# Performance work log

Measured on AMD Instinct MI355X. Metric: run time of the kernel, lower is better.

Reference implementation:

```python
import jax, jax.numpy as jnp
import numpy as np

K = 2
HD = 1024
IN = 784
NPARAMS = K + 2**K - 1  # 5
TRIL_R = np.array([0, 1, 1])  # tril_indices(2,2)
TRIL_C = np.array([0, 0, 1])


def setup_inputs() -> dict:
    key = jax.random.key(0)
    ks = jax.random.split(key, 8)
    B, T = 4096, 32
    s = 0.02
    return {
        "x": jax.random.normal(ks[0], (B, IN), jnp.float32),
        "hx": jnp.zeros((B, HD), jnp.float32),
        "eps": jax.random.normal(ks[1], (T, B, K), jnp.float32),
        "W_ih": jax.random.normal(ks[2], (HD, IN), jnp.float32) * s,
        "b_ih": jax.random.normal(ks[3], (HD,), jnp.float32) * s,
        "W_hh": jax.random.normal(ks[4], (HD, HD), jnp.float32) * s,
        "b_hh": jax.random.normal(ks[5], (HD,), jnp.float32) * s,
        "fe_W": jax.random.normal(ks[6], (NPARAMS, HD), jnp.float32) * s,
        "fe_b": jax.random.normal(ks[7], (NPARAMS,), jnp.float32) * s,
        "num_ticks": T,
    }


def _forward(x, hx, eps, W_ih, b_ih, W_hh, b_hh, fe_W, fe_b):
    B = x.shape[0]
    x_proj = x @ W_ih.T + b_ih  # invariant across ticks: [B, HD]
    diag = jnp.arange(K)

    def step(h, eps_t):
        h = jnp.tanh(x_proj + h @ W_hh.T + b_hh)  # RNNCell
        fe = h @ fe_W.T + fe_b                    # [B, NPARAMS]
        mus = fe[:, :K]
        sigmas = fe[:, K:]
        L = jnp.zeros((B, K, K), fe.dtype).at[:, TRIL_R, TRIL_C].set(sigmas)
        L = L.at[:, diag, diag].set(jax.nn.softplus(L[:, diag, diag]))
        z = mus + jnp.einsum('bij,bj->bi', L, eps_t)  # reparameterized sample
        return h, (z, L)

    _, (zs, Ls) = jax.lax.scan(step, hx, eps)  # zs: [T,B,K], Ls: [T,B,K,K]
    zs = jnp.transpose(zs, (1, 2, 0))          # [B, K, T]
    Ls = jnp.transpose(Ls, (1, 2, 3, 0))       # [B, K, K, T]
    # NOTE: original code stacks all_zs for both `zs` and `mus` (faithful to source).
    return zs, zs, Ls


def reference(x, hx, eps, W_ih, b_ih, W_hh, b_hh, fe_W, fe_b, num_ticks):
    eps = eps[:num_ticks]
    return _forward(x, hx, eps, W_ih, b_ih, W_hh, b_hh, fe_W, fe_b)
```

## Files before the change

### kernel.cpp

```cpp
#include <hip/hip_runtime.h>
#include <hip/hip_bf16.h>
#include <stdint.h>

#define B_ROWS 4096
#define HD 1024
#define IN_DIM 784
#define IN_PAD 832
#define NEXT 1152
#define T_TICKS 32

typedef float f32x4 __attribute__((ext_vector_type(4)));
typedef short short8 __attribute__((ext_vector_type(8)));
typedef __hip_bfloat16 bf16;

__device__ __forceinline__ float b2f(short s) {
  unsigned u = ((unsigned)(unsigned short)s) << 16;
  float f; __builtin_memcpy(&f, &u, 4); return f;
}

__device__ __forceinline__ float softplus_f(float x) {
  if (x > 20.f) return x;
  return log1pf(expf(x));
}

__device__ __forceinline__ float tanh_fast(float x) {
  x = fminf(fmaxf(x, -15.f), 15.f);
  float e = __expf(2.f * x);
  return (e - 1.f) / (e + 1.f);
}

__device__ __forceinline__ void gload_lds16(const void* g, void* l) {
  __builtin_amdgcn_global_load_lds(
      (const __attribute__((address_space(1))) uint32_t*)g,
      (__attribute__((address_space(3))) uint32_t*)l, 16, 0, 0);
}

__global__ __launch_bounds__(256) void conv_pad_kernel(
    const float* __restrict__ src, bf16* __restrict__ dst,
    int rows, int scols, int dcols) {
  int idx = blockIdx.x * 256 + threadIdx.x;
  int total = rows * dcols;
  if (idx >= total) return;
  int r = idx / dcols, c = idx - r * dcols;
  float v = (c < scols) ? src[(size_t)r * scols + c] : 0.f;
  dst[idx] = __float2bfloat16(v);
}

__global__ __launch_bounds__(256) void build_whhext(
    const float* __restrict__ Whh, const float* __restrict__ feW,
    bf16* __restrict__ dst) {
  int idx = blockIdx.x * 256 + threadIdx.x;
  if (idx >= NEXT * HD) return;
  int r = idx / HD, c = idx - r * HD;
  float v = 0.f;
  if (r < HD) v = Whh[(size_t)r * HD + c];
  else if (r < HD + 5) v = feW[(size_t)(r - HD) * HD + c];
  dst[idx] = __float2bfloat16(v);
}

template<int KDIM, int MODE, int NT>
__global__ __launch_bounds__(256) void gemm_bt(
    const bf16* __restrict__ A, int ldaB,
    const bf16* __restrict__ Bw, int ldbB,
    const float* __restrict__ bias1, const float* __restrict__ bias2,
    const bf16* __restrict__ xp, bf16* __restrict__ xp_out,
    bf16* __restrict__ outH, float* __restrict__ feRaw, int tprev)
{
  __shared__ bf16 lA[2][64 * 64];
  __shared__ bf16 lB[2][128 * 64];
  const int tid = threadIdx.x;
  const int lane = tid & 63, w = tid >> 6;
  const int wm = w & 1, wn = w >> 1;
  const int l3 = lane >> 3, l7 = lane & 7;
  const int gcol = l7 ^ l3;
  const int r = lane & 15, q = lane >> 4;
  const int r7 = r & 7;

  int bid = blockIdx.x;
  int mx, ny;
  if (NT == 8) {
    int v = (bid & 7) * 64 + (bid >> 3);
    mx = v >> 3; ny = v & 7;
  } else {
    int v = (bid & 7) * 72 + (bid >> 3);
    mx = v / 9; ny = v - mx * 9;
  }
  const int bm0 = mx * 64, bn0 = ny * 128;

  f32x4 acc[2][4] = {};

  const char* Asrc = (const char*)A + (size_t)(bm0 + l3) * ldaB + gcol * 16;
  const char* Bsrc = (const char*)Bw + (size_t)(bn0 + l3) * ldbB + gcol * 16;
  char* lAb0 = (char*)&lA[0][0];
  char* lBb0 = (char*)&lB[0][0];

  const int NK = KDIM / 64;

#define STAGE(buf, kt)                                                         \
  {                                                                            \
    const char* Ak = Asrc + (kt) * 128;                                        \
    const char* Bk = Bsrc + (kt) * 128;                                        \
    _Pragma("unroll") for (int j = 0; j < 2; ++j) {                            \
      int iA = w * 2 + j;                                                      \
      gload_lds16(Ak + (size_t)iA * 8 * ldaB, lAb0 + (buf) * 8192 + iA * 1024);\
    }                                                                          \
    _Pragma("unroll") for (int j = 0; j < 4; ++j) {                            \
      int iB = w * 4 + j;                                                      \
      gload_lds16(Bk + (size_t)iB * 8 * ldbB, lBb0 + (buf) * 16384 + iB * 1024);\
    }                                                                          \
  }

  STAGE(0, 0);
  int cur = 0;

  for (int kt = 0; kt < NK; ++kt) {
    if (kt + 1 < NK) {
      STAGE(cur ^ 1, kt + 1);
      asm volatile("s_waitcnt vmcnt(6)" ::: "memory");
    } else {
      asm volatile("s_waitcnt vmcnt(0)" ::: "memory");
    }
    __builtin_amdgcn_s_barrier();

    const char* lAb = lAb0 + cur * 8192;
    const char* lBb = lBb0 + cur * 16384;
    short8 af[2][2], bfr[2][4];
#pragma unroll
    for (int ks = 0; ks < 2; ++ks) {
      int cc = ks * 4 + q;
      int sw = (cc ^ r7) << 4;
#pragma unroll
      for (int m = 0; m < 2; ++m) {
        int row = wm * 32 + m * 16 + r;
        af[ks][m] = *(const short8*)(lAb + row * 128 + sw);
      }
#pragma unroll
      for (int n = 0; n < 4; ++n) {
        int row = wn * 64 + n * 16 + r;
        bfr[ks][n] = *(const short8*)(lBb + row * 128 + sw);
      }
    }
    asm volatile("s_waitcnt lgkmcnt(0)" ::: "memory");
    __builtin_amdgcn_s_barrier();
    __builtin_amdgcn_sched_barrier(0);

#pragma unroll
    for (int ks = 0; ks < 2; ++ks)
#pragma unroll
      for (int m = 0; m < 2; ++m)
#pragma unroll
        for (int n = 0; n < 4; ++n)
          acc[m][n] = __builtin_amdgcn_mfma_f32_16x16x32_bf16(af[ks][m], bfr[ks][n], acc[m][n], 0, 0, 0);

    cur ^= 1;
  }
#undef STAGE

#pragma unroll
  for (int m = 0; m < 2; ++m) {
#pragma unroll
    for (int n = 0; n < 4; ++n) {
      int coll = wn * 64 + n * 16 + r;
      int col = bn0 + coll;
#pragma unroll
      for (int i = 0; i < 4; ++i) {
        int row = bm0 + wm * 32 + m * 16 + q * 4 + i;
        float v = acc[m][n][i];
        if (MODE == 0) {
          xp_out[(size_t)row * HD + col] = __float2bfloat16(v + bias1[col] + bias2[col]);
        } else {
          if (NT == 9 && ny == 8) {
            if (coll < 5 && tprev >= 0)
              feRaw[((size_t)row * T_TICKS + tprev) * 5 + coll] = v;
          } else {
            float val = tanh_fast(v + b2f(*(const short*)&xp[(size_t)row * HD + col]));
            outH[(size_t)row * HD + col] = __float2bfloat16(val);
          }
        }
      }
    }
  }
}

__global__ __launch_bounds__(256) void fe_last(
    const bf16* __restrict__ h, const float* __restrict__ feW,
    float* __restrict__ feRaw)
{
  int wid = threadIdx.x >> 6, lane = threadIdx.x & 63;
  int b = blockIdx.x * 4 + wid;
  const bf16* hr = h + (size_t)b * HD + lane * 16;
  short8 hv0 = *(const short8*)hr;
  short8 hv1 = *(const short8*)(hr + 8);
  float hvf[16];
#pragma unroll
  for (int e = 0; e < 8; ++e) { hvf[e] = b2f(hv0[e]); hvf[8 + e] = b2f(hv1[e]); }

  float a0 = 0, a1 = 0, a2 = 0, a3 = 0, a4 = 0;
  int col0 = lane * 16;
#pragma unroll
  for (int e = 0; e < 16; ++e) {
    float hv = hvf[e];
    int col = col0 + e;
    a0 += hv * feW[0 * HD + col];
    a1 += hv * feW[1 * HD + col];
    a2 += hv * feW[2 * HD + col];
    a3 += hv * feW[3 * HD + col];
    a4 += hv * feW[4 * HD + col];
  }
#pragma unroll
  for (int off = 32; off >= 1; off >>= 1) {
    a0 += __shfl_xor(a0, off);
    a1 += __shfl_xor(a1, off);
    a2 += __shfl_xor(a2, off);
    a3 += __shfl_xor(a3, off);
    a4 += __shfl_xor(a4, off);
  }
  if (lane == 0) {
    float* fr = feRaw + ((size_t)b * T_TICKS + (T_TICKS - 1)) * 5;
    fr[0] = a0; fr[1] = a1; fr[2] = a2; fr[3] = a3; fr[4] = a4;
  }
}

__global__ __launch_bounds__(256) void finish_kernel(
    const float* __restrict__ feRaw, const float* __restrict__ feB,
    const float* __restrict__ eps, float* __restrict__ out)
{
  int gid = blockIdx.x * 256 + threadIdx.x;
  if (gid >= B_ROWS * T_TICKS) return;
  int b = gid >> 5, t = gid & 31;
  const float* fr = feRaw + ((size_t)b * T_TICKS + t) * 5;
  float mu0 = fr[0] + feB[0], mu1 = fr[1] + feB[1];
  float L00 = softplus_f(fr[2] + feB[2]);
  float L10 = fr[3] + feB[3];
  float L11 = softplus_f(fr[4] + feB[4]);
  const float* ep = eps + ((size_t)t * B_ROWS + b) * 2;
  float e0 = ep[0], e1 = ep[1];
  float z0 = mu0 + L00 * e0;
  float z1 = mu1 + L10 * e0 + L11 * e1;

  float* zs0 = out;
  float* zs1 = out + (size_t)B_ROWS * 2 * T_TICKS;
  float* Ls  = out + (size_t)2 * B_ROWS * 2 * T_TICKS;
  size_t zb = (size_t)b * 2 * T_TICKS + t;
  zs0[zb] = z0; zs0[zb + T_TICKS] = z1;
  zs1[zb] = z0; zs1[zb + T_TICKS] = z1;
  size_t lb = (size_t)b * 4 * T_TICKS + t;
  Ls[lb] = L00;
  Ls[lb + T_TICKS] = 0.f;
  Ls[lb + 2 * T_TICKS] = L10;
  Ls[lb + 3 * T_TICKS] = L11;
}

extern "C" void kernel_launch(void* const* d_in, const int* in_sizes, int n_in,
                              void* d_out, int out_size, void* d_ws, size_t ws_size,
                              hipStream_t stream) {
  const float* x    = (const float*)d_in[0];
  const float* hx   = (const float*)d_in[1];
  const float* eps  = (const float*)d_in[2];
  const float* W_ih = (const float*)d_in[3];
  const float* b_ih = (const float*)d_in[4];
  const float* W_hh = (const float*)d_in[5];
  const float* b_hh = (const float*)d_in[6];
  const float* fe_W = (const float*)d_in[7];
  const float* fe_b = (const float*)d_in[8];
  float* out = (float*)d_out;

  char* ws = (char*)d_ws;
  bf16* x_bf    = (bf16*)ws;  ws += (size_t)B_ROWS * IN_PAD * 2;
  bf16* wih_bf  = (bf16*)ws;  ws += (size_t)HD * IN_PAD * 2;
  bf16* whhe_bf = (bf16*)ws;  ws += (size_t)NEXT * HD * 2;
  bf16* xp_bf   = (bf16*)ws;  ws += (size_t)B_ROWS * HD * 2;
  bf16* hA = (bf16*)ws;       ws += (size_t)B_ROWS * HD * 2;
  bf16* hB = (bf16*)ws;       ws += (size_t)B_ROWS * HD * 2;
  float* feRaw = (float*)ws;  ws += (size_t)B_ROWS * T_TICKS * 5 * 4;

  conv_pad_kernel<<<(B_ROWS * IN_PAD + 255) / 256, 256, 0, stream>>>(x, x_bf, B_ROWS, IN_DIM, IN_PAD);
  conv_pad_kernel<<<(HD * IN_PAD + 255) / 256, 256, 0, stream>>>(W_ih, wih_bf, HD, IN_DIM, IN_PAD);
  build_whhext<<<(NEXT * HD + 255) / 256, 256, 0, stream>>>(W_hh, fe_W, whhe_bf);
  conv_pad_kernel<<<(B_ROWS * HD + 255) / 256, 256, 0, stream>>>(hx, hA, B_ROWS, HD, HD);

  gemm_bt<IN_PAD, 0, 8><<<512, 256, 0, stream>>>(
      x_bf, IN_PAD * 2, wih_bf, IN_PAD * 2, b_ih, b_hh,
      nullptr, xp_bf, nullptr, nullptr, -1);

  for (int t = 0; t < T_TICKS; ++t) {
    const bf16* hin = (t & 1) ? hB : hA;
    bf16* hout      = (t & 1) ? hA : hB;
    gemm_bt<HD, 1, 9><<<576, 256, 0, stream>>>(
        hin, HD * 2, whhe_bf, HD * 2, nullptr, nullptr,
        xp_bf, nullptr, hout, feRaw, t - 1);
  }
  fe_last<<<B_ROWS / 4, 256, 0, stream>>>(hA, fe_W, feRaw);
  finish_kernel<<<(B_ROWS * T_TICKS + 255) / 256, 256, 0, stream>>>(feRaw, fe_b, eps, out);
}
```

Before: 720.0 us.

## Fold fe projection into wave 0 of per-tick GEMM and triple-buffer LDS

The extra ninth column tile that computed the fe projection as a padded GEMM block is removed. Wave 0 of the blocks with ny<4 now does a small 16x16 MFMA against a padded fe_W tile, reusing the A tile already in LDS, so each tick launches 512 blocks instead of 576. The K loop also moves from double to triple buffering, with two stages kept in flight. The cost is more LDS per block, which may lower occupancy, plus extra load and MFMA work on wave 0 of half the blocks.

Result: faster. 576.8 us (-19.9%).

```diff
diff --git a/kernel.cpp b/kernel.cpp
--- a/kernel.cpp
+++ b/kernel.cpp
@@ -6,12 +6,15 @@
 #define HD 1024
 #define IN_DIM 784
 #define IN_PAD 832
-#define NEXT 1152
 #define T_TICKS 32
 
 typedef float f32x4 __attribute__((ext_vector_type(4)));
 typedef short short8 __attribute__((ext_vector_type(8)));
 typedef __hip_bfloat16 bf16;
+
+#define BUF_SZ 24576
+#define FEW_OFF (3 * BUF_SZ)
+#define LDS_TOTAL (3 * BUF_SZ + 3 * 2048)
 
 __device__ __forceinline__ float b2f(short s) {
   unsigned u = ((unsigned)(unsigned short)s) << 16;
@@ -46,28 +49,31 @@
   dst[idx] = __float2bfloat16(v);
 }
 
-__global__ __launch_bounds__(256) void build_whhext(
+__global__ __launch_bounds__(256) void build_wext(
     const float* __restrict__ Whh, const float* __restrict__ feW,
-    bf16* __restrict__ dst) {
+    bf16* __restrict__ whh_bf, bf16* __restrict__ feWp) {
   int idx = blockIdx.x * 256 + threadIdx.x;
-  if (idx >= NEXT * HD) return;
+  if (idx >= (HD + 16) * HD) return;
   int r = idx / HD, c = idx - r * HD;
-  float v = 0.f;
-  if (r < HD) v = Whh[(size_t)r * HD + c];
-  else if (r < HD + 5) v = feW[(size_t)(r - HD) * HD + c];
-  dst[idx] = __float2bfloat16(v);
-}
-
-template<int KDIM, int MODE, int NT>
+  if (r < HD) {
+    whh_bf[idx] = __float2bfloat16(Whh[(size_t)r * HD + c]);
+  } else {
+    int fr = r - HD;
+    float v = (fr < 5) ? feW[(size_t)fr * HD + c] : 0.f;
+    feWp[(size_t)fr * HD + c] = __float2bfloat16(v);
+  }
+}
+
+template<int KDIM, int MODE>
 __global__ __launch_bounds__(256) void gemm_bt(
-    const bf16* __restrict__ A, int ldaB,
-    const bf16* __restrict__ Bw, int ldbB,
+    const bf16* __restrict__ A,
+    const bf16* __restrict__ Bw,
+    const bf16* __restrict__ feWp,
     const float* __restrict__ bias1, const float* __restrict__ bias2,
     const bf16* __restrict__ xp, bf16* __restrict__ xp_out,
     bf16* __restrict__ outH, float* __restrict__ feRaw, int tprev)
 {
-  __shared__ bf16 lA[2][64 * 64];
-  __shared__ bf16 lB[2][128 * 64];
+  __shared__ char lds[LDS_TOTAL];
   const int tid = threadIdx.x;
   const int lane = tid & 63, w = tid >> 6;
   const int wm = w & 1, wn = w >> 1;
@@ -75,56 +81,69 @@
   const int gcol = l7 ^ l3;
   const int r = lane & 15, q = lane >> 4;
   const int r7 = r & 7;
+  const int ldaB = KDIM * 2, ldbB = KDIM * 2;
 
   int bid = blockIdx.x;
-  int mx, ny;
-  if (NT == 8) {
-    int v = (bid & 7) * 64 + (bid >> 3);
-    mx = v >> 3; ny = v & 7;
-  } else {
-    int v = (bid & 7) * 72 + (bid >> 3);
-    mx = v / 9; ny = v - mx * 9;
-  }
+  int v = (bid & 7) * 64 + (bid >> 3);
+  const int mx = v >> 3, ny = v & 7;
   const int bm0 = mx * 64, bn0 = ny * 128;
 
+  const bool feB = (MODE == 1) && (ny < 4);
+  const bool feW0 = feB && (w == 0);
+
   f32x4 acc[2][4] = {};
+  f32x4 acc_fe = {};
 
   const char* Asrc = (const char*)A + (size_t)(bm0 + l3) * ldaB + gcol * 16;
   const char* Bsrc = (const char*)Bw + (size_t)(bn0 + l3) * ldbB + gcol * 16;
-  char* lAb0 = (char*)&lA[0][0];
-  char* lBb0 = (char*)&lB[0][0];
+  const char* Fsrc = (const char*)feWp + (size_t)l3 * 2048 + gcol * 16;
 
   const int NK = KDIM / 64;
 
-#define STAGE(buf, kt)                                                         \
-  {                                                                            \
-    const char* Ak = Asrc + (kt) * 128;                                        \
-    const char* Bk = Bsrc + (kt) * 128;                                        \
-    _Pragma("unroll") for (int j = 0; j < 2; ++j) {                            \
-      int iA = w * 2 + j;                                                      \
-      gload_lds16(Ak + (size_t)iA * 8 * ldaB, lAb0 + (buf) * 8192 + iA * 1024);\
-    }                                                                          \
-    _Pragma("unroll") for (int j = 0; j < 4; ++j) {                            \
-      int iB = w * 4 + j;                                                      \
-      gload_lds16(Bk + (size_t)iB * 8 * ldbB, lBb0 + (buf) * 16384 + iB * 1024);\
-    }                                                                          \
+#define STAGE(buf, kt)                                                          \
+  {                                                                             \
+    const char* Ak = Asrc + (kt) * 128;                                         \
+    const char* Bk = Bsrc + (kt) * 128;                                         \
+    _Pragma("unroll") for (int j = 0; j < 2; ++j) {                             \
+      int iA = w * 2 + j;                                                       \
+      gload_lds16(Ak + (size_t)iA * 8 * ldaB, lds + (buf) * BUF_SZ + iA * 1024);\
+    }                                                                           \
+    _Pragma("unroll") for (int j = 0; j < 4; ++j) {                             \
+      int iB = w * 4 + j;                                                       \
+      gload_lds16(Bk + (size_t)iB * 8 * ldbB,                                   \
+                  lds + (buf) * BUF_SZ + 8192 + iB * 1024);                     \
+    }                                                                           \
+    if (feW0) {                                                                 \
+      const char* Fk = Fsrc + (kt) * 128;                                       \
+      _Pragma("unroll") for (int j = 0; j < 2; ++j) {                           \
+        gload_lds16(Fk + (size_t)j * 8 * 2048,                                  \
+                    lds + FEW_OFF + (buf) * 2048 + j * 1024);                   \
+      }                                                                         \
+    }                                                                           \
   }
 
   STAGE(0, 0);
-  int cur = 0;
+  STAGE(1, 1);
+  int b0 = 0;
 
   for (int kt = 0; kt < NK; ++kt) {
-    if (kt + 1 < NK) {
-      STAGE(cur ^ 1, kt + 1);
-      asm volatile("s_waitcnt vmcnt(6)" ::: "memory");
+    int bs = b0 + 2; if (bs >= 3) bs -= 3;
+    if (kt + 2 < NK) {
+      STAGE(bs, kt + 2);
+      if (feW0) asm volatile("s_waitcnt vmcnt(16)" ::: "memory");
+      else      asm volatile("s_waitcnt vmcnt(12)" ::: "memory");
+    } else if (kt + 2 == NK) {
+      if (feW0) asm volatile("s_waitcnt vmcnt(8)" ::: "memory");
+      else      asm volatile("s_waitcnt vmcnt(6)" ::: "memory");
     } else {
       asm volatile("s_waitcnt vmcnt(0)" ::: "memory");
     }
     __builtin_amdgcn_s_barrier();
-
-    const char* lAb = lAb0 + cur * 8192;
-    const char* lBb = lBb0 + cur * 16384;
-    short8 af[2][2], bfr[2][4];
+    __builtin_amdgcn_sched_barrier(0);
+
+    const char* lAb = lds + b0 * BUF_SZ;
+    const char* lBb = lAb + 8192;
+    short8 af[2][2], bfr[2][4], af_fe[2], bf_fe[2];
 #pragma unroll
     for (int ks = 0; ks < 2; ++ks) {
       int cc = ks * 4 + q;
@@ -140,6 +159,15 @@
         bfr[ks][n] = *(const short8*)(lBb + row * 128 + sw);
       }
     }
+    if (feW0) {
+      const char* lFb = lds + FEW_OFF + b0 * 2048;
+#pragma unroll
+      for (int ks = 0; ks < 2; ++ks) {
+        int sw = ((ks * 4 + q) ^ r7) << 4;
+        af_fe[ks] = *(const short8*)(lAb + (ny * 16 + r) * 128 + sw);
+        bf_fe[ks] = *(const short8*)(lFb + r * 128 + sw);
+      }
+    }
     asm volatile("s_waitcnt lgkmcnt(0)" ::: "memory");
     __builtin_amdgcn_s_barrier();
     __builtin_amdgcn_sched_barrier(0);
@@ -151,8 +179,12 @@
 #pragma unroll
         for (int n = 0; n < 4; ++n)
           acc[m][n] = __builtin_amdgcn_mfma_f32_16x16x32_bf16(af[ks][m], bfr[ks][n], acc[m][n], 0, 0, 0);
-
-    cur ^= 1;
+    if (feW0) {
+      acc_fe = __builtin_amdgcn_mfma_f32_16x16x32_bf16(af_fe[0], bf_fe[0], acc_fe, 0, 0, 0);
+      acc_fe = __builtin_amdgcn_mfma_f32_16x16x32_bf16(af_fe[1], bf_fe[1], acc_fe, 0, 0, 0);
+    }
+
+    if (++b0 == 3) b0 = 0;
   }
 #undef STAGE
 
@@ -160,24 +192,25 @@
   for (int m = 0; m < 2; ++m) {
 #pragma unroll
     for (int n = 0; n < 4; ++n) {
-      int coll = wn * 64 + n * 16 + r;
-      int col = bn0 + coll;
+      int col = bn0 + wn * 64 + n * 16 + r;
 #pragma unroll
       for (int i = 0; i < 4; ++i) {
         int row = bm0 + wm * 32 + m * 16 + q * 4 + i;
-        float v = acc[m][n][i];
+        float vv = acc[m][n][i];
         if (MODE == 0) {
-          xp_out[(size_t)row * HD + col] = __float2bfloat16(v + bias1[col] + bias2[col]);
+          xp_out[(size_t)row * HD + col] = __float2bfloat16(vv + bias1[col] + bias2[col]);
         } else {
-          if (NT == 9 && ny == 8) {
-            if (coll < 5 && tprev >= 0)
-              feRaw[((size_t)row * T_TICKS + tprev) * 5 + coll] = v;
-          } else {
-            float val = tanh_fast(v + b2f(*(const short*)&xp[(size_t)row * HD + col]));
-            outH[(size_t)row * HD + col] = __float2bfloat16(val);
-          }
+          float val = tanh_fast(vv + b2f(*(const short*)&xp[(size_t)row * HD + col]));
+          outH[(size_t)row * HD + col] = __float2bfloat16(val);
         }
       }
+    }
+  }
+  if (MODE == 1 && feW0 && tprev >= 0 && r < 5) {
+#pragma unroll
+    for (int i = 0; i < 4; ++i) {
+      int rowg = bm0 + ny * 16 + q * 4 + i;
+      feRaw[((size_t)rowg * T_TICKS + tprev) * 5 + r] = acc_fe[i];
     }
   }
 }
@@ -268,7 +301,8 @@
   char* ws = (char*)d_ws;
   bf16* x_bf    = (bf16*)ws;  ws += (size_t)B_ROWS * IN_PAD * 2;
   bf16* wih_bf  = (bf16*)ws;  ws += (size_t)HD * IN_PAD * 2;
-  bf16* whhe_bf = (bf16*)ws;  ws += (size_t)NEXT * HD * 2;
+  bf16* whh_bf  = (bf16*)ws;  ws += (size_t)HD * HD * 2;
+  bf16* feWp    = (bf16*)ws;  ws += (size_t)16 * HD * 2;
   bf16* xp_bf   = (bf16*)ws;  ws += (size_t)B_ROWS * HD * 2;
   bf16* hA = (bf16*)ws;       ws += (size_t)B_ROWS * HD * 2;
   bf16* hB = (bf16*)ws;       ws += (size_t)B_ROWS * HD * 2;
@@ -276,18 +310,18 @@
 
   conv_pad_kernel<<<(B_ROWS * IN_PAD + 255) / 256, 256, 0, stream>>>(x, x_bf, B_ROWS, IN_DIM, IN_PAD);
   conv_pad_kernel<<<(HD * IN_PAD + 255) / 256, 256, 0, stream>>>(W_ih, wih_bf, HD, IN_DIM, IN_PAD);
-  build_whhext<<<(NEXT * HD + 255) / 256, 256, 0, stream>>>(W_hh, fe_W, whhe_bf);
+  build_wext<<<((HD + 16) * HD + 255) / 256, 256, 0, stream>>>(W_hh, fe_W, whh_bf, feWp);
   conv_pad_kernel<<<(B_ROWS * HD + 255) / 256, 256, 0, stream>>>(hx, hA, B_ROWS, HD, HD);
 
-  gemm_bt<IN_PAD, 0, 8><<<512, 256, 0, stream>>>(
-      x_bf, IN_PAD * 2, wih_bf, IN_PAD * 2, b_ih, b_hh,
+  gemm_bt<IN_PAD, 0><<<512, 256, 0, stream>>>(
+      x_bf, wih_bf, nullptr, b_ih, b_hh,
       nullptr, xp_bf, nullptr, nullptr, -1);
 
   for (int t = 0; t < T_TICKS; ++t) {
     const bf16* hin = (t & 1) ? hB : hA;
     bf16* hout      = (t & 1) ? hA : hB;
-    gemm_bt<HD, 1, 9><<<576, 256, 0, stream>>>(
-        hin, HD * 2, whhe_bf, HD * 2, nullptr, nullptr,
+    gemm_bt<HD, 1><<<512, 256, 0, stream>>>(
+        hin, whh_bf, feWp, nullptr, nullptr,
         xp_bf, nullptr, hout, feRaw, t - 1);
   }
   fe_last<<<B_ROWS / 4, 256, 0, stream>>>(hA, fe_W, feRaw);
```

## Pre-pack weights into MFMA fragment layout and load B directly to registers

Applied to the files above, without the earlier changes.

Weights are repacked once into an MFMA-fragment-ordered layout so each wave loads its B operands straight from global memory into registers with coalesced 16-byte loads, double-buffered two k-steps ahead, and only the A tile goes through LDS. The extra 9th column tile that computed the 5 fe outputs is removed. The fe projection is now done by wave 0 of blocks with ny<4 using a small packed fe weight block and one extra MFMA pair per k-step, so the recurrent launch drops from 576 to 512 blocks. This cuts LDS traffic and footprint and removes a mostly-wasted tile, at the cost of more register pressure and heavier global/L2 reads for B.

Result: faster. 631.5 us (-12.3%).

```diff
diff --git a/kernel.cpp b/kernel.cpp
--- a/kernel.cpp
+++ b/kernel.cpp
@@ -6,12 +6,13 @@
 #define HD 1024
 #define IN_DIM 784
 #define IN_PAD 832
-#define NEXT 1152
 #define T_TICKS 32
 
 typedef float f32x4 __attribute__((ext_vector_type(4)));
 typedef short short8 __attribute__((ext_vector_type(8)));
 typedef __hip_bfloat16 bf16;
+
+#define ABUF 8192
 
 __device__ __forceinline__ float b2f(short s) {
   unsigned u = ((unsigned)(unsigned short)s) << 16;
@@ -46,28 +47,61 @@
   dst[idx] = __float2bfloat16(v);
 }
 
-__global__ __launch_bounds__(256) void build_whhext(
-    const float* __restrict__ Whh, const float* __restrict__ feW,
-    bf16* __restrict__ dst) {
-  int idx = blockIdx.x * 256 + threadIdx.x;
-  if (idx >= NEXT * HD) return;
-  int r = idx / HD, c = idx - r * HD;
-  float v = 0.f;
-  if (r < HD) v = Whh[(size_t)r * HD + c];
-  else if (r < HD + 5) v = feW[(size_t)(r - HD) * HD + c];
-  dst[idx] = __float2bfloat16(v);
-}
-
-template<int KDIM, int MODE, int NT>
-__global__ __launch_bounds__(256) void gemm_bt(
-    const bf16* __restrict__ A, int ldaB,
-    const bf16* __restrict__ Bw, int ldbB,
+__global__ __launch_bounds__(256) void pack_w(
+    const float* __restrict__ src, bf16* __restrict__ dst,
+    int nkt, int scols) {
+  int gid = blockIdx.x * 256 + threadIdx.x;
+  int lane = gid & 63, f = gid >> 6;
+  int total = 16 * nkt * 2 * 4;
+  if (f >= total) return;
+  int n = f & 3;
+  int rest = f >> 2;
+  int ks = rest & 1;
+  int rest2 = rest >> 1;
+  int kt = rest2 % nkt;
+  int wnny = rest2 / nkt;
+  int r = lane & 15, q = lane >> 4;
+  int row = wnny * 64 + n * 16 + r;
+  int k0 = kt * 64 + ks * 32 + q * 8;
+  short8 v;
+#pragma unroll
+  for (int e = 0; e < 8; ++e) {
+    int c = k0 + e;
+    float x = (c < scols) ? src[(size_t)row * scols + c] : 0.f;
+    bf16 b = __float2bfloat16(x);
+    v[e] = *(short*)&b;
+  }
+  *(short8*)((char*)dst + (size_t)f * 1024 + lane * 16) = v;
+}
+
+__global__ __launch_bounds__(256) void pack_fe(
+    const float* __restrict__ feW, bf16* __restrict__ dst) {
+  int gid = blockIdx.x * 256 + threadIdx.x;
+  int lane = gid & 63, f = gid >> 6;
+  if (f >= 32) return;
+  int ks = f & 1, kt = f >> 1;
+  int r = lane & 15, q = lane >> 4;
+  int k0 = kt * 64 + ks * 32 + q * 8;
+  short8 v;
+#pragma unroll
+  for (int e = 0; e < 8; ++e) {
+    float x = (r < 5) ? feW[(size_t)r * HD + k0 + e] : 0.f;
+    bf16 b = __float2bfloat16(x);
+    v[e] = *(short*)&b;
+  }
+  *(short8*)((char*)dst + (size_t)f * 1024 + lane * 16) = v;
+}
+
+template<int KDIM, int MODE>
+__global__ __launch_bounds__(256) void gemm_core(
+    const bf16* __restrict__ A,
+    const bf16* __restrict__ Bpk,
+    const bf16* __restrict__ feP,
     const float* __restrict__ bias1, const float* __restrict__ bias2,
     const bf16* __restrict__ xp, bf16* __restrict__ xp_out,
     bf16* __restrict__ outH, float* __restrict__ feRaw, int tprev)
 {
-  __shared__ bf16 lA[2][64 * 64];
-  __shared__ bf16 lB[2][128 * 64];
+  __shared__ char lds[2 * ABUF];
   const int tid = threadIdx.x;
   const int lane = tid & 63, w = tid >> 6;
   const int wm = w & 1, wn = w >> 1;
@@ -75,109 +109,116 @@
   const int gcol = l7 ^ l3;
   const int r = lane & 15, q = lane >> 4;
   const int r7 = r & 7;
+  const int lane16 = lane * 16;
+  const int ldaB = KDIM * 2;
+  const int NK = KDIM / 64;
 
   int bid = blockIdx.x;
-  int mx, ny;
-  if (NT == 8) {
-    int v = (bid & 7) * 64 + (bid >> 3);
-    mx = v >> 3; ny = v & 7;
-  } else {
-    int v = (bid & 7) * 72 + (bid >> 3);
-    mx = v / 9; ny = v - mx * 9;
-  }
+  int v = (bid & 7) * 64 + (bid >> 3);
+  const int mx = v >> 3, ny = v & 7;
   const int bm0 = mx * 64, bn0 = ny * 128;
 
+  const bool feW0 = (MODE == 1) && (ny < 4) && (w == 0);
+
   f32x4 acc[2][4] = {};
+  f32x4 acc_fe = {};
 
   const char* Asrc = (const char*)A + (size_t)(bm0 + l3) * ldaB + gcol * 16;
-  const char* Bsrc = (const char*)Bw + (size_t)(bn0 + l3) * ldbB + gcol * 16;
-  char* lAb0 = (char*)&lA[0][0];
-  char* lBb0 = (char*)&lB[0][0];
-
-  const int NK = KDIM / 64;
-
-#define STAGE(buf, kt)                                                         \
+  const char* Bkt  = (const char*)Bpk + (size_t)(ny * 2 + wn) * NK * 8192;
+
+  short8 Be[8], Bo[8], Bef[2], Bof[2];
+
+#define STAGEA(buf, k)                                                         \
   {                                                                            \
-    const char* Ak = Asrc + (kt) * 128;                                        \
-    const char* Bk = Bsrc + (kt) * 128;                                        \
+    const char* Ak = Asrc + (size_t)(k) * 128;                                 \
     _Pragma("unroll") for (int j = 0; j < 2; ++j) {                            \
       int iA = w * 2 + j;                                                      \
-      gload_lds16(Ak + (size_t)iA * 8 * ldaB, lAb0 + (buf) * 8192 + iA * 1024);\
-    }                                                                          \
-    _Pragma("unroll") for (int j = 0; j < 4; ++j) {                            \
-      int iB = w * 4 + j;                                                      \
-      gload_lds16(Bk + (size_t)iB * 8 * ldbB, lBb0 + (buf) * 16384 + iB * 1024);\
-    }                                                                          \
-  }
-
-  STAGE(0, 0);
-  int cur = 0;
-
-  for (int kt = 0; kt < NK; ++kt) {
-    if (kt + 1 < NK) {
-      STAGE(cur ^ 1, kt + 1);
-      asm volatile("s_waitcnt vmcnt(6)" ::: "memory");
-    } else {
-      asm volatile("s_waitcnt vmcnt(0)" ::: "memory");
-    }
-    __builtin_amdgcn_s_barrier();
-
-    const char* lAb = lAb0 + cur * 8192;
-    const char* lBb = lBb0 + cur * 16384;
-    short8 af[2][2], bfr[2][4];
-#pragma unroll
-    for (int ks = 0; ks < 2; ++ks) {
-      int cc = ks * 4 + q;
-      int sw = (cc ^ r7) << 4;
-#pragma unroll
-      for (int m = 0; m < 2; ++m) {
-        int row = wm * 32 + m * 16 + r;
-        af[ks][m] = *(const short8*)(lAb + row * 128 + sw);
-      }
-#pragma unroll
-      for (int n = 0; n < 4; ++n) {
-        int row = wn * 64 + n * 16 + r;
-        bfr[ks][n] = *(const short8*)(lBb + row * 128 + sw);
+      gload_lds16(Ak + (size_t)iA * 8 * ldaB, lds + (buf) * ABUF + iA * 1024); \
+    }                                                                          \
+  }
+
+#define ISSUEB(BS, BSf, k)                                                     \
+  {                                                                            \
+    const char* bp = Bkt + (size_t)(k) * 8192;                                 \
+    _Pragma("unroll") for (int i = 0; i < 8; ++i)                              \
+      BS[i] = *(const short8*)(bp + i * 1024 + lane16);                        \
+    if (feW0) {                                                                \
+      const char* fp = (const char*)feP + (size_t)(k) * 2048;                  \
+      BSf[0] = *(const short8*)(fp + lane16);                                  \
+      BSf[1] = *(const short8*)(fp + 1024 + lane16);                           \
+    }                                                                          \
+  }
+
+#define ITER(kp, BS, BSf)                                                      \
+  {                                                                            \
+    const int _k = (kp);                                                       \
+    if (_k + 1 < NK) STAGEA((_k + 1) & 1, _k + 1);                             \
+    const char* lAb = lds + (_k & 1) * ABUF;                                   \
+    short8 af[2][2], af_fe[2];                                                 \
+    _Pragma("unroll") for (int ks = 0; ks < 2; ++ks) {                         \
+      int sw = ((ks * 4 + q) ^ r7) << 4;                                       \
+      _Pragma("unroll") for (int m = 0; m < 2; ++m)                            \
+        af[ks][m] = *(const short8*)(lAb + (wm * 32 + m * 16 + r) * 128 + sw); \
+    }                                                                          \
+    if (feW0) {                                                                \
+      _Pragma("unroll") for (int ks = 0; ks < 2; ++ks) {                       \
+        int sw = ((ks * 4 + q) ^ r7) << 4;                                     \
+        af_fe[ks] = *(const short8*)(lAb + (ny * 16 + r) * 128 + sw);          \
+      }                                                                        \
+    }                                                                          \
+    _Pragma("unroll") for (int ks = 0; ks < 2; ++ks)                           \
+      _Pragma("unroll") for (int m = 0; m < 2; ++m)                            \
+        _Pragma("unroll") for (int n = 0; n < 4; ++n)                          \
+          acc[m][n] = __builtin_amdgcn_mfma_f32_16x16x32_bf16(                 \
+              af[ks][m], BS[ks * 4 + n], acc[m][n], 0, 0, 0);                  \
+    if (feW0) {                                                                \
+      acc_fe = __builtin_amdgcn_mfma_f32_16x16x32_bf16(af_fe[0], BSf[0], acc_fe, 0, 0, 0); \
+      acc_fe = __builtin_amdgcn_mfma_f32_16x16x32_bf16(af_fe[1], BSf[1], acc_fe, 0, 0, 0); \
+    }                                                                          \
+    if (_k + 2 < NK) ISSUEB(BS, BSf, _k + 2);                                  \
+    __syncthreads();                                                           \
+  }
+
+  STAGEA(0, 0);
+  ISSUEB(Be, Bef, 0);
+  ISSUEB(Bo, Bof, 1);
+  __syncthreads();
+
+#pragma unroll
+  for (int kt = 0; kt + 1 < NK; kt += 2) {
+    ITER(kt,     Be, Bef);
+    ITER(kt + 1, Bo, Bof);
+  }
+  if (NK & 1) {
+    ITER(NK - 1, Be, Bef);
+  }
+#undef ITER
+#undef ISSUEB
+#undef STAGEA
+
+#pragma unroll
+  for (int m = 0; m < 2; ++m) {
+#pragma unroll
+    for (int n = 0; n < 4; ++n) {
+      int col = bn0 + wn * 64 + n * 16 + r;
+#pragma unroll
+      for (int i = 0; i < 4; ++i) {
+        int row = bm0 + wm * 32 + m * 16 + q * 4 + i;
+        float vv = acc[m][n][i];
+        if (MODE == 0) {
+          xp_out[(size_t)row * HD + col] = __float2bfloat16(vv + bias1[col] + bias2[col]);
+        } else {
+          float val = tanh_fast(vv + b2f(*(const short*)&xp[(size_t)row * HD + col]));
+          outH[(size_t)row * HD + col] = __float2bfloat16(val);
+        }
       }
     }
-    asm volatile("s_waitcnt lgkmcnt(0)" ::: "memory");
-    __builtin_amdgcn_s_barrier();
-    __builtin_amdgcn_sched_barrier(0);
-
-#pragma unroll
-    for (int ks = 0; ks < 2; ++ks)
-#pragma unroll
-      for (int m = 0; m < 2; ++m)
-#pragma unroll
-        for (int n = 0; n < 4; ++n)
-          acc[m][n] = __builtin_amdgcn_mfma_f32_16x16x32_bf16(af[ks][m], bfr[ks][n], acc[m][n], 0, 0, 0);
-
-    cur ^= 1;
-  }
-#undef STAGE
-
-#pragma unroll
-  for (int m = 0; m < 2; ++m) {
-#pragma unroll
-    for (int n = 0; n < 4; ++n) {
-      int coll = wn * 64 + n * 16 + r;
-      int col = bn0 + coll;
-#pragma unroll
-      for (int i = 0; i < 4; ++i) {
-        int row = bm0 + wm * 32 + m * 16 + q * 4 + i;
-        float v = acc[m][n][i];
-        if (MODE == 0) {
-          xp_out[(size_t)row * HD + col] = __float2bfloat16(v + bias1[col] + bias2[col]);
-        } else {
-          if (NT == 9 && ny == 8) {
-            if (coll < 5 && tprev >= 0)
-              feRaw[((size_t)row * T_TICKS + tprev) * 5 + coll] = v;
-          } else {
-            float val = tanh_fast(v + b2f(*(const short*)&xp[(size_t)row * HD + col]));
-            outH[(size_t)row * HD + col] = __float2bfloat16(val);
-          }
-        }
-      }
+  }
+  if (feW0 && tprev >= 0 && r < 5) {
+#pragma unroll
+    for (int i = 0; i < 4; ++i) {
+      int rowg = bm0 + ny * 16 + q * 4 + i;
+      feRaw[((size_t)rowg * T_TICKS + tprev) * 5 + r] = acc_fe[i];
     }
   }
 }
@@ -265,29 +306,36 @@
   const float* fe_b = (const float*)d_in[8];
   float* out = (float*)d_out;
 
+  const int NKT_HH = HD / 64;
+  const int NKT_IH = IN_PAD / 64;
+  const int FR_HH = 16 * NKT_HH * 2 * 4;
+  const int FR_IH = 16 * NKT_IH * 2 * 4;
+
   char* ws = (char*)d_ws;
   bf16* x_bf    = (bf16*)ws;  ws += (size_t)B_ROWS * IN_PAD * 2;
-  bf16* wih_bf  = (bf16*)ws;  ws += (size_t)HD * IN_PAD * 2;
-  bf16* whhe_bf = (bf16*)ws;  ws += (size_t)NEXT * HD * 2;
+  bf16* hA      = (bf16*)ws;  ws += (size_t)B_ROWS * HD * 2;
+  bf16* hB      = (bf16*)ws;  ws += (size_t)B_ROWS * HD * 2;
   bf16* xp_bf   = (bf16*)ws;  ws += (size_t)B_ROWS * HD * 2;
-  bf16* hA = (bf16*)ws;       ws += (size_t)B_ROWS * HD * 2;
-  bf16* hB = (bf16*)ws;       ws += (size_t)B_ROWS * HD * 2;
-  float* feRaw = (float*)ws;  ws += (size_t)B_ROWS * T_TICKS * 5 * 4;
+  bf16* pk_hh   = (bf16*)ws;  ws += (size_t)FR_HH * 1024;
+  bf16* pk_ih   = (bf16*)ws;  ws += (size_t)FR_IH * 1024;
+  bf16* feP     = (bf16*)ws;  ws += (size_t)32 * 1024;
+  float* feRaw  = (float*)ws; ws += (size_t)B_ROWS * T_TICKS * 5 * 4;
 
   conv_pad_kernel<<<(B_ROWS * IN_PAD + 255) / 256, 256, 0, stream>>>(x, x_bf, B_ROWS, IN_DIM, IN_PAD);
-  conv_pad_kernel<<<(HD * IN_PAD + 255) / 256, 256, 0, stream>>>(W_ih, wih_bf, HD, IN_DIM, IN_PAD);
-  build_whhext<<<(NEXT * HD + 255) / 256, 256, 0, stream>>>(W_hh, fe_W, whhe_bf);
   conv_pad_kernel<<<(B_ROWS * HD + 255) / 256, 256, 0, stream>>>(hx, hA, B_ROWS, HD, HD);
-
-  gemm_bt<IN_PAD, 0, 8><<<512, 256, 0, stream>>>(
-      x_bf, IN_PAD * 2, wih_bf, IN_PAD * 2, b_ih, b_hh,
+  pack_w<<<(FR_HH * 64 + 255) / 256, 256, 0, stream>>>(W_hh, pk_hh, NKT_HH, HD);
+  pack_w<<<(FR_IH * 64 + 255) / 256, 256, 0, stream>>>(W_ih, pk_ih, NKT_IH, IN_DIM);
+  pack_fe<<<(32 * 64 + 255) / 256, 256, 0, stream>>>(fe_W, feP);
+
+  gemm_core<IN_PAD, 0><<<512, 256, 0, stream>>>(
+      x_bf, pk_ih, nullptr, b_ih, b_hh,
       nullptr, xp_bf, nullptr, nullptr, -1);
 
   for (int t = 0; t < T_TICKS; ++t) {
     const bf16* hin = (t & 1) ? hB : hA;
     bf16* hout      = (t & 1) ? hA : hB;
-    gemm_bt<HD, 1, 9><<<576, 256, 0, stream>>>(
-        hin, HD * 2, whhe_bf, HD * 2, nullptr, nullptr,
+    gemm_core<HD, 1><<<512, 256, 0, stream>>>(
+        hin, pk_hh, feP, nullptr, nullptr,
         xp_bf, nullptr, hout, feRaw, t - 1);
   }
   fe_last<<<B_ROWS / 4, 256, 0, stream>>>(hA, fe_W, feRaw);
```
